# Performance work log

Hardware: AMD Instinct MI355X
Metric: run time of the kernel (lower is better)

Reference implementation:

```python
import jax, jax.numpy as jnp
import numpy as np

N_NODES = 100000
N_EDGES = 2000000
N_GRAPHS = 1000
DIM = 32
NUM_FEATURES = 7
NUM_CLASSES = 2
BN_EPS = 1e-5


def setup_inputs() -> dict:
    key = jax.random.key(0)
    ks = jax.random.split(key, 24)
    inp = {
        "x": jax.random.normal(ks[0], (N_NODES, NUM_FEATURES), dtype=jnp.float32),
        "edge_index": jax.random.randint(ks[1], (2, N_EDGES), 0, N_NODES, dtype=jnp.int64),
        "batch": jnp.sort(jax.random.randint(ks[2], (N_NODES,), 0, N_GRAPHS, dtype=jnp.int64)),
        "conv1_W1": jax.random.normal(ks[3], (NUM_FEATURES, DIM), dtype=jnp.float32) * 0.3,
        "conv1_b1": jax.random.normal(ks[4], (DIM,), dtype=jnp.float32) * 0.1,
        "conv1_W2": jax.random.normal(ks[5], (DIM, DIM), dtype=jnp.float32) * 0.15,
        "conv1_b2": jax.random.normal(ks[6], (DIM,), dtype=jnp.float32) * 0.1,
        "convs_W1": jax.random.normal(ks[7], (4, DIM, DIM), dtype=jnp.float32) * 0.15,
        "convs_b1": jax.random.normal(ks[8], (4, DIM), dtype=jnp.float32) * 0.1,
        "convs_W2": jax.random.normal(ks[9], (4, DIM, DIM), dtype=jnp.float32) * 0.15,
        "convs_b2": jax.random.normal(ks[10], (4, DIM), dtype=jnp.float32) * 0.1,
        "bn_gamma": jax.random.uniform(ks[11], (5, DIM), dtype=jnp.float32, minval=0.5, maxval=1.5),
        "bn_beta": jax.random.normal(ks[12], (5, DIM), dtype=jnp.float32) * 0.1,
        "bn_mean": jax.random.normal(ks[13], (5, DIM), dtype=jnp.float32) * 0.1,
        "bn_var": jax.random.uniform(ks[14], (5, DIM), dtype=jnp.float32, minval=0.5, maxval=1.5),
        "fc1_W": jax.random.normal(ks[15], (DIM, DIM), dtype=jnp.float32) * 0.15,
        "fc1_b": jax.random.normal(ks[16], (DIM,), dtype=jnp.float32) * 0.1,
        "fc2_W": jax.random.normal(ks[17], (DIM, NUM_CLASSES), dtype=jnp.float32) * 0.15,
        "fc2_b": jax.random.normal(ks[18], (NUM_CLASSES,), dtype=jnp.float32) * 0.1,
    }
    return inp


def _gin_conv(h, src, dst, W1, b1, W2, b2):
    # GINConv with eps=0: nn((1+eps)*x + sum_{j in N(i)} x_j)
    agg = jax.ops.segment_sum(h[src], dst, num_segments=N_NODES)
    z = h + agg
    z = jnp.maximum(z @ W1 + b1, 0.0)
    return z @ W2 + b2


def _bn_eval(h, gamma, beta, mean, var):
    return (h - mean) * jax.lax.rsqrt(var + BN_EPS) * gamma + beta


def reference(x, edge_index, batch,
              conv1_W1, conv1_b1, conv1_W2, conv1_b2,
              convs_W1, convs_b1, convs_W2, convs_b2,
              bn_gamma, bn_beta, bn_mean, bn_var,
              fc1_W, fc1_b, fc2_W, fc2_b):
    src, dst = edge_index[0], edge_index[1]
    h = _gin_conv(x, src, dst, conv1_W1, conv1_b1, conv1_W2, conv1_b2)
    h = jnp.maximum(h, 0.0)
    h = _bn_eval(h, bn_gamma[0], bn_beta[0], bn_mean[0], bn_var[0])
    for i in range(4):  # conv2..conv5
        h = _gin_conv(h, src, dst, convs_W1[i], convs_b1[i], convs_W2[i], convs_b2[i])
        h = jnp.maximum(h, 0.0)
        h = _bn_eval(h, bn_gamma[i + 1], bn_beta[i + 1], bn_mean[i + 1], bn_var[i + 1])
    # global add pool over graphs
    g = jax.ops.segment_sum(h, batch, num_segments=N_GRAPHS)  # [G, DIM]
    g = jnp.maximum(g @ fc1_W + fc1_b, 0.0)
    # dropout: eval mode -> identity
    logits = g @ fc2_W + fc2_b
    return jax.nn.log_softmax(logits, axis=-1)
```

## Files before the change

### kernel.cpp

```cpp
#include <hip/hip_runtime.h>

#define N_NODES  100000
#define N_EDGES  2000000
#define N_GRAPHS 1000
#define NFEAT    7
#define BN_EPS   1e-5f
#define MAXDEG   64

#define BSH      7
#define NBKT     782
#define BCAP     3584
#define E_PER_BLK 4096
#define NGRP     6250

__device__ __forceinline__ unsigned bf16_rne(float f) {
  unsigned u = __float_as_uint(f);
  return (u + 0x7FFFu + ((u >> 16) & 1u)) >> 16;
}
__device__ __forceinline__ float bf_lo(unsigned u) { return __uint_as_float(u << 16); }
__device__ __forceinline__ float bf_hi(unsigned u) { return __uint_as_float(u & 0xFFFF0000u); }

typedef __bf16 bf16x8 __attribute__((ext_vector_type(8)));
typedef float  f32x4  __attribute__((ext_vector_type(4)));

__global__ __launch_bounds__(1024) void b1_bucket(const int* __restrict__ src,
                                                  const int* __restrict__ dst,
                                                  int* __restrict__ gCur,
                                                  unsigned* __restrict__ ebuf) {
  __shared__ int hist[NBKT], base[NBKT];
  int tid = threadIdx.x;
  for (int i = tid; i < NBKT; i += 1024) hist[i] = 0;
  __syncthreads();
  unsigned pk[4];
  int bo[4];
  int e0 = blockIdx.x * E_PER_BLK;
#pragma unroll
  for (int k = 0; k < 4; ++k) {
    int e = e0 + k * 1024 + tid;
    if (e < N_EDGES) {
      int d = dst[e], s = src[e];
      int b = d >> BSH;
      int off = atomicAdd(&hist[b], 1);
      pk[k] = ((unsigned)(d & 127) << 17) | (unsigned)s;
      bo[k] = (b << 17) | off;
    } else {
      bo[k] = -1;
    }
  }
  __syncthreads();
  for (int i = tid; i < NBKT; i += 1024)
    base[i] = hist[i] ? atomicAdd(&gCur[i], hist[i]) : 0;
  __syncthreads();
#pragma unroll
  for (int k = 0; k < 4; ++k) {
    if (bo[k] >= 0) {
      int b = bo[k] >> 17, off = bo[k] & 0x1FFFF;
      int p = base[b] + off;
      if (p < BCAP) ebuf[(size_t)b * BCAP + p] = pk[k];
    }
  }
}

__global__ __launch_bounds__(512) void b2_csr(const unsigned* __restrict__ ebuf,
                                              const int* __restrict__ gCnt,
                                              int* __restrict__ cnt,
                                              int* __restrict__ csr,
                                              int* __restrict__ gmax) {
  __shared__ int hist[128];
  __shared__ int stage[128 * MAXDEG];
  int b = blockIdx.x, tid = threadIdx.x;
  if (tid < 128) hist[tid] = 0;
  for (int i = tid; i < 128 * MAXDEG; i += 512) stage[i] = (b << BSH) + (i >> 6);
  __syncthreads();
  int n = gCnt[b];
  if (n > BCAP) n = BCAP;
  const unsigned* eb = ebuf + (size_t)b * BCAP;
  for (int i = tid; i < n; i += 512) {
    unsigned pk = eb[i];
    int dloc = (int)(pk >> 17);
    int slot = atomicAdd(&hist[dloc], 1);
    if (slot < MAXDEG) stage[(dloc << 6) + slot] = (int)(pk & 0x1FFFFu);
  }
  __syncthreads();
  if (tid < 128) {
    int gnode = (b << BSH) + tid;
    if (gnode < N_NODES) cnt[gnode] = hist[tid];
  }
  if (tid < 8) {
    int mx = 1;
#pragma unroll
    for (int k = 0; k < 16; ++k) {
      int d = hist[tid * 16 + k];
      if (d > 63) d = 63;
      if (d + 1 > mx) mx = d + 1;
    }
    gmax[(b << 3) + tid] = mx;
  }
  const int4* st4 = (const int4*)stage;
  int4* dst4 = (int4*)(csr + (size_t)b * (128 * MAXDEG));
  for (int i = tid; i < 128 * MAXDEG / 4; i += 512) dst4[i] = st4[i];
}

__global__ __launch_bounds__(256) void xcvt_kernel(const float* __restrict__ x,
                                                   unsigned* __restrict__ xc) {
  int i = blockIdx.x * 256 + threadIdx.x;
  if (i >= N_NODES * 4) return;
  int n = i >> 2, p = i & 3;
  float lo = x[n * 7 + 2 * p];
  float hi = (2 * p + 1 < 7) ? x[n * 7 + 2 * p + 1] : 0.f;
  xc[i] = bf16_rne(lo) | (bf16_rne(hi) << 16);
}

__global__ __launch_bounds__(256) void gin1(
    const unsigned short* __restrict__ xc16, const int* __restrict__ cnt,
    const int* __restrict__ csr, const int* __restrict__ gmax,
    const float* __restrict__ W1, const float* __restrict__ b1,
    const float* __restrict__ W2, const float* __restrict__ b2,
    const float* __restrict__ gamma, const float* __restrict__ beta,
    const float* __restrict__ mean, const float* __restrict__ var,
    unsigned short* __restrict__ hout16) {
  __shared__ __align__(16) float zs[4][16][12];
  __shared__ __align__(16) float ts[4][32];
  int tid = threadIdx.x;
  int w = __builtin_amdgcn_readfirstlane(tid >> 6);
  int lane = tid & 63;
  int nl = lane & 15;
  int c  = lane >> 4;
  int half = lane >> 5, j = lane & 31;

  float wr1[4], wr2[16];
#pragma unroll
  for (int i = 0; i < 4; ++i) {
    int k = half * 4 + i;
    wr1[i] = (k < 7) ? W1[k * 32 + j] : 0.f;
  }
#pragma unroll
  for (int i = 0; i < 16; ++i) wr2[i] = W2[(half * 16 + i) * 32 + j];
  float vb1 = b1[j], vb2 = b2[j];
  float sc = gamma[j] * rsqrtf(var[j] + BN_EPS);
  float sh = beta[j] - mean[j] * sc;

  const unsigned* xc32 = (const unsigned*)xc16;

  const int NW = gridDim.x * 4;
  for (int g = blockIdx.x * 4 + w; g < NGRP; g += NW) {
    int node = g * 16 + nl;
    int dcnt = cnt[node];
    if (dcnt > 63) dcnt = 63;
    int dE = dcnt + 1;
    int dmax = __builtin_amdgcn_readfirstlane(gmax[g]);
    int nb = (dmax + 3) >> 2;

    const int* crow = csr + (size_t)node * MAXDEG;
    float a0 = 0.f, a1 = 0.f;

    uint4 i4 = *(const uint4*)crow;
    for (int b = 0; b < nb; ++b) {
      uint4 i4n = i4;
      if (b + 1 < nb) i4n = *(const uint4*)(crow + (b + 1) * 4);
      unsigned v0 = xc32[(size_t)i4.x * 4 + c];
      unsigned v1 = xc32[(size_t)i4.y * 4 + c];
      unsigned v2 = xc32[(size_t)i4.z * 4 + c];
      unsigned v3 = xc32[(size_t)i4.w * 4 + c];
      int s0 = b * 4;
      if (s0 + 0 < dE) { a0 += bf_lo(v0); a1 += bf_hi(v0); }
      if (s0 + 1 < dE) { a0 += bf_lo(v1); a1 += bf_hi(v1); }
      if (s0 + 2 < dE) { a0 += bf_lo(v2); a1 += bf_hi(v2); }
      if (s0 + 3 < dE) { a0 += bf_lo(v3); a1 += bf_hi(v3); }
      i4 = i4n;
    }

    {
      float2 z0 = {a0, a1};
      *(float2*)&zs[w][nl][c * 2] = z0;
    }

    for (int p = 0; p < 16; ++p) {
      int np = g * 16 + p;
      float tp = half ? 0.f : vb1;
      {
        const float4* zp = (const float4*)&zs[w][p][half * 4];
        float4 z0 = zp[0];
        tp = fmaf(z0.x, wr1[0], tp); tp = fmaf(z0.y, wr1[1], tp);
        tp = fmaf(z0.z, wr1[2], tp); tp = fmaf(z0.w, wr1[3], tp);
      }
      tp += __shfl_xor(tp, 32);
      tp = fmaxf(tp, 0.f);
      if (!half) ts[w][j] = tp;

      float op = half ? 0.f : vb2;
      {
        const float4* tpp = (const float4*)&ts[w][half * 16];
        float4 t0 = tpp[0], t1 = tpp[1], t2 = tpp[2], t3 = tpp[3];
        op = fmaf(t0.x, wr2[0], op);  op = fmaf(t0.y, wr2[1], op);
        op = fmaf(t0.z, wr2[2], op);  op = fmaf(t0.w, wr2[3], op);
        op = fmaf(t1.x, wr2[4], op);  op = fmaf(t1.y, wr2[5], op);
        op = fmaf(t1.z, wr2[6], op);  op = fmaf(t1.w, wr2[7], op);
        op = fmaf(t2.x, wr2[8], op);  op = fmaf(t2.y, wr2[9], op);
        op = fmaf(t2.z, wr2[10], op); op = fmaf(t2.w, wr2[11], op);
        op = fmaf(t3.x, wr2[12], op); op = fmaf(t3.y, wr2[13], op);
        op = fmaf(t3.z, wr2[14], op); op = fmaf(t3.w, wr2[15], op);
      }
      op += __shfl_xor(op, 32);
      if (!half) {
        op = fmaxf(op, 0.f) * sc + sh;
        float hi = __shfl(op, j | 1);
        if ((j & 1) == 0) {
          unsigned pk = bf16_rne(op) | (bf16_rne(hi) << 16);
          ((unsigned*)hout16)[np * 16 + (j >> 1)] = pk;
        }
      }
    }
  }
}

__global__ __launch_bounds__(256) void gin_layer32(
    const unsigned short* __restrict__ hin16, const int* __restrict__ cnt,
    const int* __restrict__ csr, const int* __restrict__ gmax,
    const float* __restrict__ W1, const float* __restrict__ b1,
    const float* __restrict__ W2, const float* __restrict__ b2,
    const float* __restrict__ gamma, const float* __restrict__ beta,
    const float* __restrict__ mean, const float* __restrict__ var,
    unsigned short* __restrict__ hout16) {
  __shared__ __align__(16) float ts[4][16][36];
  int tid = threadIdx.x;
  int w = __builtin_amdgcn_readfirstlane(tid >> 6);
  int lane = tid & 63;
  int nl = lane & 15;
  int q  = lane >> 4;

  bf16x8 w1ah, w1al, w1bh, w1bl, w2ah, w2al, w2bh, w2bl;
#pragma unroll
  for (int i = 0; i < 8; ++i) {
    float f;
    __bf16 h;
    f = W1[(q * 8 + i) * 32 + nl];       h = (__bf16)f;
    w1ah[i] = h; w1al[i] = (__bf16)(f - (float)h);
    f = W1[(q * 8 + i) * 32 + 16 + nl];  h = (__bf16)f;
    w1bh[i] = h; w1bl[i] = (__bf16)(f - (float)h);
    f = W2[(q * 8 + i) * 32 + nl];       h = (__bf16)f;
    w2ah[i] = h; w2al[i] = (__bf16)(f - (float)h);
    f = W2[(q * 8 + i) * 32 + 16 + nl];  h = (__bf16)f;
    w2bh[i] = h; w2bl[i] = (__bf16)(f - (float)h);
  }
  float vb1a = b1[nl], vb1b = b1[16 + nl];
  float vb2a = b2[nl], vb2b = b2[16 + nl];
  f32x4 cb1a = {vb1a, vb1a, vb1a, vb1a};
  f32x4 cb1b = {vb1b, vb1b, vb1b, vb1b};
  f32x4 cb2a = {vb2a, vb2a, vb2a, vb2a};
  f32x4 cb2b = {vb2b, vb2b, vb2b, vb2b};
  float sc0 = gamma[nl] * rsqrtf(var[nl] + BN_EPS);
  float sh0 = beta[nl] - mean[nl] * sc0;
  float sc1 = gamma[16 + nl] * rsqrtf(var[16 + nl] + BN_EPS);
  float sh1 = beta[16 + nl] - mean[16 + nl] * sc1;

  const int NW = gridDim.x * 4;
  for (int g = blockIdx.x * 4 + w; g < NGRP; g += NW) {
    int node = g * 16 + nl;
    int dcnt = cnt[node];
    if (dcnt > 63) dcnt = 63;
    int dE = dcnt + 1;
    int dmax = __builtin_amdgcn_readfirstlane(gmax[g]);
    int nb = (dmax + 3) >> 2;

    const int* crow = csr + (size_t)node * MAXDEG;
    float acc[8];
#pragma unroll
    for (int i = 0; i < 8; ++i) acc[i] = 0.f;

    uint4 iA = *(const uint4*)crow;
    uint4 r0 = *(const uint4*)(hin16 + (size_t)iA.x * 32 + q * 8);
    uint4 r1 = *(const uint4*)(hin16 + (size_t)iA.y * 32 + q * 8);
    uint4 r2 = *(const uint4*)(hin16 + (size_t)iA.z * 32 + q * 8);
    uint4 r3 = *(const uint4*)(hin16 + (size_t)iA.w * 32 + q * 8);
    uint4 iB = iA;
    if (nb > 1) iB = *(const uint4*)(crow + 4);

    for (int b = 0; b < nb; ++b) {
      bool hasN = (b + 1 < nb);
      uint4 n0 = r0, n1 = r1, n2 = r2, n3 = r3;
      if (hasN) {
        n0 = *(const uint4*)(hin16 + (size_t)iB.x * 32 + q * 8);
        n1 = *(const uint4*)(hin16 + (size_t)iB.y * 32 + q * 8);
        n2 = *(const uint4*)(hin16 + (size_t)iB.z * 32 + q * 8);
        n3 = *(const uint4*)(hin16 + (size_t)iB.w * 32 + q * 8);
      }
      uint4 iC = iB;
      if (b + 2 < nb) iC = *(const uint4*)(crow + (b + 2) * 4);

      int s0 = b * 4;
      if (s0 + 0 < dE) {
        acc[0] += bf_lo(r0.x); acc[1] += bf_hi(r0.x);
        acc[2] += bf_lo(r0.y); acc[3] += bf_hi(r0.y);
        acc[4] += bf_lo(r0.z); acc[5] += bf_hi(r0.z);
        acc[6] += bf_lo(r0.w); acc[7] += bf_hi(r0.w);
      }
      if (s0 + 1 < dE) {
        acc[0] += bf_lo(r1.x); acc[1] += bf_hi(r1.x);
        acc[2] += bf_lo(r1.y); acc[3] += bf_hi(r1.y);
        acc[4] += bf_lo(r1.z); acc[5] += bf_hi(r1.z);
        acc[6] += bf_lo(r1.w); acc[7] += bf_hi(r1.w);
      }
      if (s0 + 2 < dE) {
        acc[0] += bf_lo(r2.x); acc[1] += bf_hi(r2.x);
        acc[2] += bf_lo(r2.y); acc[3] += bf_hi(r2.y);
        acc[4] += bf_lo(r2.z); acc[5] += bf_hi(r2.z);
        acc[6] += bf_lo(r2.w); acc[7] += bf_hi(r2.w);
      }
      if (s0 + 3 < dE) {
        acc[0] += bf_lo(r3.x); acc[1] += bf_hi(r3.x);
        acc[2] += bf_lo(r3.y); acc[3] += bf_hi(r3.y);
        acc[4] += bf_lo(r3.z); acc[5] += bf_hi(r3.z);
        acc[6] += bf_lo(r3.w); acc[7] += bf_hi(r3.w);
      }
      r0 = n0; r1 = n1; r2 = n2; r3 = n3;
      iB = iC;
    }

    bf16x8 af, afl;
#pragma unroll
    for (int i = 0; i < 8; ++i) {
      __bf16 h = (__bf16)acc[i];
      af[i] = h;
      afl[i] = (__bf16)(acc[i] - (float)h);
    }

    f32x4 t0 = __builtin_amdgcn_mfma_f32_16x16x32_bf16(af,  w1ah, cb1a, 0, 0, 0);
    t0 = __builtin_amdgcn_mfma_f32_16x16x32_bf16(afl, w1ah, t0, 0, 0, 0);
    t0 = __builtin_amdgcn_mfma_f32_16x16x32_bf16(af,  w1al, t0, 0, 0, 0);
    f32x4 t1 = __builtin_amdgcn_mfma_f32_16x16x32_bf16(af,  w1bh, cb1b, 0, 0, 0);
    t1 = __builtin_amdgcn_mfma_f32_16x16x32_bf16(afl, w1bh, t1, 0, 0, 0);
    t1 = __builtin_amdgcn_mfma_f32_16x16x32_bf16(af,  w1bl, t1, 0, 0, 0);
#pragma unroll
    for (int r = 0; r < 4; ++r) {
      t0[r] = fmaxf(t0[r], 0.f);
      t1[r] = fmaxf(t1[r], 0.f);
    }
#pragma unroll
    for (int r = 0; r < 4; ++r) {
      ts[w][q * 4 + r][nl]      = t0[r];
      ts[w][q * 4 + r][16 + nl] = t1[r];
    }
    bf16x8 af2, af2l;
    {
      float4 r0f = *(const float4*)&ts[w][nl][q * 8];
      float4 r1f = *(const float4*)&ts[w][nl][q * 8 + 4];
      float tv[8] = {r0f.x, r0f.y, r0f.z, r0f.w, r1f.x, r1f.y, r1f.z, r1f.w};
#pragma unroll
      for (int i = 0; i < 8; ++i) {
        __bf16 h = (__bf16)tv[i];
        af2[i] = h;
        af2l[i] = (__bf16)(tv[i] - (float)h);
      }
    }

    f32x4 o0 = __builtin_amdgcn_mfma_f32_16x16x32_bf16(af2,  w2ah, cb2a, 0, 0, 0);
    o0 = __builtin_amdgcn_mfma_f32_16x16x32_bf16(af2l, w2ah, o0, 0, 0, 0);
    o0 = __builtin_amdgcn_mfma_f32_16x16x32_bf16(af2,  w2al, o0, 0, 0, 0);
    f32x4 o1 = __builtin_amdgcn_mfma_f32_16x16x32_bf16(af2,  w2bh, cb2b, 0, 0, 0);
    o1 = __builtin_amdgcn_mfma_f32_16x16x32_bf16(af2l, w2bh, o1, 0, 0, 0);
    o1 = __builtin_amdgcn_mfma_f32_16x16x32_bf16(af2,  w2bl, o1, 0, 0, 0);
#pragma unroll
    for (int r = 0; r < 4; ++r) {
      o0[r] = fmaxf(o0[r], 0.f) * sc0 + sh0;
      o1[r] = fmaxf(o1[r], 0.f) * sc1 + sh1;
    }
#pragma unroll
    for (int r = 0; r < 4; ++r) {
      ts[w][q * 4 + r][nl]      = o0[r];
      ts[w][q * 4 + r][16 + nl] = o1[r];
    }
    {
      float4 f0 = *(const float4*)&ts[w][nl][q * 8];
      float4 f1 = *(const float4*)&ts[w][nl][q * 8 + 4];
      uint4 st;
      st.x = bf16_rne(f0.x) | (bf16_rne(f0.y) << 16);
      st.y = bf16_rne(f0.z) | (bf16_rne(f0.w) << 16);
      st.z = bf16_rne(f1.x) | (bf16_rne(f1.y) << 16);
      st.w = bf16_rne(f1.z) | (bf16_rne(f1.w) << 16);
      *(uint4*)(hout16 + (size_t)node * 32 + q * 8) = st;
    }
  }
}

__global__ __launch_bounds__(256) void pool_kernel(const unsigned short* __restrict__ h16,
                                                   const int* __restrict__ batch,
                                                   float* __restrict__ g) {
  __shared__ int s_lo, s_hi;
  __shared__ float red[8][33];
  int gr = blockIdx.x;
  if (threadIdx.x == 0) {
    int lo = 0, hi = N_NODES;
    while (lo < hi) { int m = (lo + hi) >> 1; if (batch[m] < gr) lo = m + 1; else hi = m; }
    s_lo = lo;
  } else if (threadIdx.x == 1) {
    int lo = 0, hi = N_NODES;
    while (lo < hi) { int m = (lo + hi) >> 1; if (batch[m] < gr + 1) lo = m + 1; else hi = m; }
    s_hi = lo;
  }
  __syncthreads();
  int lo = s_lo, hi = s_hi;
  int j = threadIdx.x & 31;
  int nd = threadIdx.x >> 5;
  float acc = 0.f;
  for (int n = lo + nd; n < hi; n += 8)
    acc += __uint_as_float((unsigned)h16[n * 32 + j] << 16);
  red[nd][j] = acc;
  __syncthreads();
  if (threadIdx.x < 32) {
    float s = 0.f;
#pragma unroll
    for (int r = 0; r < 8; ++r) s += red[r][j];
    g[gr * 32 + j] = s;
  }
}

__global__ __launch_bounds__(256) void head_kernel(
    const float* __restrict__ g, const float* __restrict__ W1, const float* __restrict__ b1,
    const float* __restrict__ W2, const float* __restrict__ b2, float* __restrict__ out) {
  __shared__ float sW1[1024], sb1[32];
  __shared__ float sW2[64], sb2[2];
  __shared__ float zb[8][33], tb[8][33], lb[8][2];
  int tid = threadIdx.x;
  for (int i = tid; i < 1024; i += 256) sW1[i] = W1[i];
  if (tid < 64) sW2[tid] = W2[tid];
  if (tid < 32) sb1[tid] = b1[tid];
  if (tid < 2) sb2[tid] = b2[tid];
  int nd = tid >> 5;
  int gr = blockIdx.x * 8 + nd;
  int j = tid & 31;
  __syncthreads();
  float z = (gr < N_GRAPHS) ? g[gr * 32 + j] : 0.f;
  zb[nd][j] = z;
  __syncthreads();
  float t = sb1[j];
#pragma unroll
  for (int k = 0; k < 32; ++k) t = fmaf(zb[nd][k], sW1[k * 32 + j], t);
  t = fmaxf(t, 0.f);
  tb[nd][j] = t;
  __syncthreads();
  if (j < 2) {
    float l = sb2[j];
#pragma unroll
    for (int k = 0; k < 32; ++k) l = fmaf(tb[nd][k], sW2[k * 2 + j], l);
    lb[nd][j] = l;
  }
  __syncthreads();
  if (gr < N_GRAPHS && j < 2) {
    float l0 = lb[nd][0], l1 = lb[nd][1];
    float m = fmaxf(l0, l1);
    float lse = m + logf(expf(l0 - m) + expf(l1 - m));
    out[gr * 2 + j] = lb[nd][j] - lse;
  }
}

extern "C" void kernel_launch(void* const* d_in, const int* in_sizes, int n_in,
                              void* d_out, int out_size, void* d_ws, size_t ws_size,
                              hipStream_t stream) {
  const float* x     = (const float*)d_in[0];
  const int*   eidx  = (const int*)d_in[1];
  const int*   batch = (const int*)d_in[2];
  const float* c1W1  = (const float*)d_in[3];
  const float* c1b1  = (const float*)d_in[4];
  const float* c1W2  = (const float*)d_in[5];
  const float* c1b2  = (const float*)d_in[6];
  const float* csW1  = (const float*)d_in[7];
  const float* csb1  = (const float*)d_in[8];
  const float* csW2  = (const float*)d_in[9];
  const float* csb2  = (const float*)d_in[10];
  const float* bng   = (const float*)d_in[11];
  const float* bnb   = (const float*)d_in[12];
  const float* bnm   = (const float*)d_in[13];
  const float* bnv   = (const float*)d_in[14];
  const float* fc1W  = (const float*)d_in[15];
  const float* fc1b  = (const float*)d_in[16];
  const float* fc2W  = (const float*)d_in[17];
  const float* fc2b  = (const float*)d_in[18];
  float* out = (float*)d_out;

  const int* src = eidx;
  const int* dst = eidx + N_EDGES;

  char* p = (char*)d_ws;
  unsigned short* hA16 = (unsigned short*)p; p += (size_t)N_NODES * 32 * 2;
  unsigned short* hB16 = (unsigned short*)p; p += (size_t)N_NODES * 32 * 2;
  int*      cnt  = (int*)p;      p += (size_t)N_NODES * 4;
  int*      csr  = (int*)p;      p += (size_t)NBKT * 128 * MAXDEG * 4;
  unsigned* ebuf = (unsigned*)p; p += (size_t)NBKT * BCAP * 4;
  int*      gCur = (int*)p;      p += 1024 * 4;
  int*      gmax = (int*)p;      p += (size_t)(NBKT * 8) * 4;
  float*    g    = (float*)p;    p += (size_t)N_GRAPHS * 32 * 4;
  unsigned* xc = ebuf;

  (void)hipMemsetAsync(gCur, 0, 1024 * 4, stream);
  b1_bucket<<<(N_EDGES + E_PER_BLK - 1) / E_PER_BLK, 1024, 0, stream>>>(src, dst, gCur, ebuf);
  b2_csr<<<NBKT, 512, 0, stream>>>(ebuf, gCur, cnt, csr, gmax);

  xcvt_kernel<<<(N_NODES * 4 + 255) / 256, 256, 0, stream>>>(x, xc);

  gin1<<<(NGRP + 3) / 4, 256, 0, stream>>>(
      (const unsigned short*)xc, cnt, csr, gmax, c1W1, c1b1, c1W2, c1b2,
      bng, bnb, bnm, bnv, hA16);

  unsigned short* cur = hA16;
  unsigned short* nxt = hB16;
  for (int i = 0; i < 4; ++i) {
    gin_layer32<<<(NGRP + 3) / 4, 256, 0, stream>>>(
        cur, cnt, csr, gmax,
        csW1 + (size_t)i * 1024, csb1 + (size_t)i * 32,
        csW2 + (size_t)i * 1024, csb2 + (size_t)i * 32,
        bng + (size_t)(i + 1) * 32, bnb + (size_t)(i + 1) * 32,
        bnm + (size_t)(i + 1) * 32, bnv + (size_t)(i + 1) * 32, nxt);
    unsigned short* tmp = cur; cur = nxt; nxt = tmp;
  }

  pool_kernel<<<N_GRAPHS, 256, 0, stream>>>(cur, batch, g);
  head_kernel<<<(N_GRAPHS + 7) / 8, 256, 0, stream>>>(g, fc1W, fc1b, fc2W, fc2b, out);
}
```

Before: 295.9 us.

## Use split-bf16 MFMA for gin1 MLP and prefetch gathers one batch ahead

The first GIN layer's per-node scalar FMA loop over 16 nodes is replaced by MFMA 16x16x32 bf16 matrix ops. Each operand is split into hi and lo bf16 parts so the products keep roughly fp32 accuracy. The neighbour gather loop is also software-pipelined so the feature loads for the next index batch are issued before the current batch is accumulated. This aims to cut ALU and shuffle cost in the MLP and hide gather latency, at the cost of more registers and LDS transposes.

```diff
diff --git a/kernel.cpp b/kernel.cpp
--- a/kernel.cpp
+++ b/kernel.cpp
@@ -120,25 +120,46 @@
     const float* __restrict__ mean, const float* __restrict__ var,
     unsigned short* __restrict__ hout16) {
   __shared__ __align__(16) float zs[4][16][12];
-  __shared__ __align__(16) float ts[4][32];
+  __shared__ __align__(16) float ts[4][16][36];
   int tid = threadIdx.x;
   int w = __builtin_amdgcn_readfirstlane(tid >> 6);
   int lane = tid & 63;
   int nl = lane & 15;
-  int c  = lane >> 4;
-  int half = lane >> 5, j = lane & 31;
-
-  float wr1[4], wr2[16];
-#pragma unroll
-  for (int i = 0; i < 4; ++i) {
-    int k = half * 4 + i;
-    wr1[i] = (k < 7) ? W1[k * 32 + j] : 0.f;
-  }
-#pragma unroll
-  for (int i = 0; i < 16; ++i) wr2[i] = W2[(half * 16 + i) * 32 + j];
-  float vb1 = b1[j], vb2 = b2[j];
-  float sc = gamma[j] * rsqrtf(var[j] + BN_EPS);
-  float sh = beta[j] - mean[j] * sc;
+  int q  = lane >> 4;
+
+  bf16x8 w1ah, w1al, w1bh, w1bl;
+#pragma unroll
+  for (int i = 0; i < 8; ++i) {
+    float fa = 0.f, fb = 0.f;
+    if (q == 0 && i < 7) {
+      fa = W1[i * 32 + nl];
+      fb = W1[i * 32 + 16 + nl];
+    }
+    __bf16 ha = (__bf16)fa;
+    w1ah[i] = ha; w1al[i] = (__bf16)(fa - (float)ha);
+    __bf16 hb = (__bf16)fb;
+    w1bh[i] = hb; w1bl[i] = (__bf16)(fb - (float)hb);
+  }
+  bf16x8 w2ah, w2al, w2bh, w2bl;
+#pragma unroll
+  for (int i = 0; i < 8; ++i) {
+    float f;
+    __bf16 h;
+    f = W2[(q * 8 + i) * 32 + nl];       h = (__bf16)f;
+    w2ah[i] = h; w2al[i] = (__bf16)(f - (float)h);
+    f = W2[(q * 8 + i) * 32 + 16 + nl];  h = (__bf16)f;
+    w2bh[i] = h; w2bl[i] = (__bf16)(f - (float)h);
+  }
+  float vb1a = b1[nl], vb1b = b1[16 + nl];
+  float vb2a = b2[nl], vb2b = b2[16 + nl];
+  f32x4 cb1a = {vb1a, vb1a, vb1a, vb1a};
+  f32x4 cb1b = {vb1b, vb1b, vb1b, vb1b};
+  f32x4 cb2a = {vb2a, vb2a, vb2a, vb2a};
+  f32x4 cb2b = {vb2b, vb2b, vb2b, vb2b};
+  float sc0 = gamma[nl] * rsqrtf(var[nl] + BN_EPS);
+  float sh0 = beta[nl] - mean[nl] * sc0;
+  float sc1 = gamma[16 + nl] * rsqrtf(var[16 + nl] + BN_EPS);
+  float sh1 = beta[16 + nl] - mean[16 + nl] * sc1;
 
   const unsigned* xc32 = (const unsigned*)xc16;
 
@@ -154,62 +175,108 @@
     const int* crow = csr + (size_t)node * MAXDEG;
     float a0 = 0.f, a1 = 0.f;
 
-    uint4 i4 = *(const uint4*)crow;
+    uint4 iA = *(const uint4*)crow;
+    unsigned r0 = xc32[(size_t)iA.x * 4 + q];
+    unsigned r1 = xc32[(size_t)iA.y * 4 + q];
+    unsigned r2 = xc32[(size_t)iA.z * 4 + q];
+    unsigned r3 = xc32[(size_t)iA.w * 4 + q];
+    uint4 iB = iA;
+    if (nb > 1) iB = *(const uint4*)(crow + 4);
+
     for (int b = 0; b < nb; ++b) {
-      uint4 i4n = i4;
-      if (b + 1 < nb) i4n = *(const uint4*)(crow + (b + 1) * 4);
-      unsigned v0 = xc32[(size_t)i4.x * 4 + c];
-      unsigned v1 = xc32[(size_t)i4.y * 4 + c];
-      unsigned v2 = xc32[(size_t)i4.z * 4 + c];
-      unsigned v3 = xc32[(size_t)i4.w * 4 + c];
+      bool hasN = (b + 1 < nb);
+      unsigned n0 = r0, n1 = r1, n2 = r2, n3 = r3;
+      if (hasN) {
+        n0 = xc32[(size_t)iB.x * 4 + q];
+        n1 = xc32[(size_t)iB.y * 4 + q];
+        n2 = xc32[(size_t)iB.z * 4 + q];
+        n3 = xc32[(size_t)iB.w * 4 + q];
+      }
+      uint4 iC = iB;
+      if (b + 2 < nb) iC = *(const uint4*)(crow + (b + 2) * 4);
+
       int s0 = b * 4;
-      if (s0 + 0 < dE) { a0 += bf_lo(v0); a1 += bf_hi(v0); }
-      if (s0 + 1 < dE) { a0 += bf_lo(v1); a1 += bf_hi(v1); }
-      if (s0 + 2 < dE) { a0 += bf_lo(v2); a1 += bf_hi(v2); }
-      if (s0 + 3 < dE) { a0 += bf_lo(v3); a1 += bf_hi(v3); }
-      i4 = i4n;
+      if (s0 + 0 < dE) { a0 += bf_lo(r0); a1 += bf_hi(r0); }
+      if (s0 + 1 < dE) { a0 += bf_lo(r1); a1 += bf_hi(r1); }
+      if (s0 + 2 < dE) { a0 += bf_lo(r2); a1 += bf_hi(r2); }
+      if (s0 + 3 < dE) { a0 += bf_lo(r3); a1 += bf_hi(r3); }
+      r0 = n0; r1 = n1; r2 = n2; r3 = n3;
+      iB = iC;
     }
 
     {
       float2 z0 = {a0, a1};
-      *(float2*)&zs[w][nl][c * 2] = z0;
-    }
-
-    for (int p = 0; p < 16; ++p) {
-      int np = g * 16 + p;
-      float tp = half ? 0.f : vb1;
-      {
-        const float4* zp = (const float4*)&zs[w][p][half * 4];
-        float4 z0 = zp[0];
-        tp = fmaf(z0.x, wr1[0], tp); tp = fmaf(z0.y, wr1[1], tp);
-        tp = fmaf(z0.z, wr1[2], tp); tp = fmaf(z0.w, wr1[3], tp);
-      }
-      tp += __shfl_xor(tp, 32);
-      tp = fmaxf(tp, 0.f);
-      if (!half) ts[w][j] = tp;
-
-      float op = half ? 0.f : vb2;
-      {
-        const float4* tpp = (const float4*)&ts[w][half * 16];
-        float4 t0 = tpp[0], t1 = tpp[1], t2 = tpp[2], t3 = tpp[3];
-        op = fmaf(t0.x, wr2[0], op);  op = fmaf(t0.y, wr2[1], op);
-        op = fmaf(t0.z, wr2[2], op);  op = fmaf(t0.w, wr2[3], op);
-        op = fmaf(t1.x, wr2[4], op);  op = fmaf(t1.y, wr2[5], op);
-        op = fmaf(t1.z, wr2[6], op);  op = fmaf(t1.w, wr2[7], op);
-        op = fmaf(t2.x, wr2[8], op);  op = fmaf(t2.y, wr2[9], op);
-        op = fmaf(t2.z, wr2[10], op); op = fmaf(t2.w, wr2[11], op);
-        op = fmaf(t3.x, wr2[12], op); op = fmaf(t3.y, wr2[13], op);
-        op = fmaf(t3.z, wr2[14], op); op = fmaf(t3.w, wr2[15], op);
-      }
-      op += __shfl_xor(op, 32);
-      if (!half) {
-        op = fmaxf(op, 0.f) * sc + sh;
-        float hi = __shfl(op, j | 1);
-        if ((j & 1) == 0) {
-          unsigned pk = bf16_rne(op) | (bf16_rne(hi) << 16);
-          ((unsigned*)hout16)[np * 16 + (j >> 1)] = pk;
-        }
-      }
+      *(float2*)&zs[w][nl][q * 2] = z0;
+    }
+    bf16x8 af, afl;
+#pragma unroll
+    for (int i = 0; i < 8; ++i) { af[i] = (__bf16)0.f; afl[i] = (__bf16)0.f; }
+    if (q == 0) {
+      float4 z0 = *(const float4*)&zs[w][nl][0];
+      float4 z1 = *(const float4*)&zs[w][nl][4];
+      float zv[8] = {z0.x, z0.y, z0.z, z0.w, z1.x, z1.y, z1.z, z1.w};
+#pragma unroll
+      for (int i = 0; i < 8; ++i) {
+        __bf16 h = (__bf16)zv[i];
+        af[i] = h;
+        afl[i] = (__bf16)(zv[i] - (float)h);
+      }
+    }
+
+    f32x4 t0 = __builtin_amdgcn_mfma_f32_16x16x32_bf16(af,  w1ah, cb1a, 0, 0, 0);
+    t0 = __builtin_amdgcn_mfma_f32_16x16x32_bf16(afl, w1ah, t0, 0, 0, 0);
+    t0 = __builtin_amdgcn_mfma_f32_16x16x32_bf16(af,  w1al, t0, 0, 0, 0);
+    f32x4 t1 = __builtin_amdgcn_mfma_f32_16x16x32_bf16(af,  w1bh, cb1b, 0, 0, 0);
+    t1 = __builtin_amdgcn_mfma_f32_16x16x32_bf16(afl, w1bh, t1, 0, 0, 0);
+    t1 = __builtin_amdgcn_mfma_f32_16x16x32_bf16(af,  w1bl, t1, 0, 0, 0);
+#pragma unroll
+    for (int r = 0; r < 4; ++r) {
+      t0[r] = fmaxf(t0[r], 0.f);
+      t1[r] = fmaxf(t1[r], 0.f);
+    }
+#pragma unroll
+    for (int r = 0; r < 4; ++r) {
+      ts[w][q * 4 + r][nl]      = t0[r];
+      ts[w][q * 4 + r][16 + nl] = t1[r];
+    }
+    bf16x8 af2, af2l;
+    {
+      float4 r0f = *(const float4*)&ts[w][nl][q * 8];
+      float4 r1f = *(const float4*)&ts[w][nl][q * 8 + 4];
+      float tv[8] = {r0f.x, r0f.y, r0f.z, r0f.w, r1f.x, r1f.y, r1f.z, r1f.w};
+#pragma unroll
+      for (int i = 0; i < 8; ++i) {
+        __bf16 h = (__bf16)tv[i];
+        af2[i] = h;
+        af2l[i] = (__bf16)(tv[i] - (float)h);
+      }
+    }
+
+    f32x4 o0 = __builtin_amdgcn_mfma_f32_16x16x32_bf16(af2,  w2ah, cb2a, 0, 0, 0);
+    o0 = __builtin_amdgcn_mfma_f32_16x16x32_bf16(af2l, w2ah, o0, 0, 0, 0);
+    o0 = __builtin_amdgcn_mfma_f32_16x16x32_bf16(af2,  w2al, o0, 0, 0, 0);
+    f32x4 o1 = __builtin_amdgcn_mfma_f32_16x16x32_bf16(af2,  w2bh, cb2b, 0, 0, 0);
+    o1 = __builtin_amdgcn_mfma_f32_16x16x32_bf16(af2l, w2bh, o1, 0, 0, 0);
+    o1 = __builtin_amdgcn_mfma_f32_16x16x32_bf16(af2,  w2bl, o1, 0, 0, 0);
+#pragma unroll
+    for (int r = 0; r < 4; ++r) {
+      o0[r] = fmaxf(o0[r], 0.f) * sc0 + sh0;
+      o1[r] = fmaxf(o1[r], 0.f) * sc1 + sh1;
+    }
+#pragma unroll
+    for (int r = 0; r < 4; ++r) {
+      ts[w][q * 4 + r][nl]      = o0[r];
+      ts[w][q * 4 + r][16 + nl] = o1[r];
+    }
+    {
+      float4 f0 = *(const float4*)&ts[w][nl][q * 8];
+      float4 f1 = *(const float4*)&ts[w][nl][q * 8 + 4];
+      uint4 st;
+      st.x = bf16_rne(f0.x) | (bf16_rne(f0.y) << 16);
+      st.y = bf16_rne(f0.z) | (bf16_rne(f0.w) << 16);
+      st.z = bf16_rne(f1.x) | (bf16_rne(f1.y) << 16);
+      st.w = bf16_rne(f1.z) | (bf16_rne(f1.w) << 16);
+      *(uint4*)(hout16 + (size_t)node * 32 + q * 8) = st;
     }
   }
 }
```

Measured after the change: 293.4 us. About the same (-0.9%).
